# Kernel tuning notes

Hardware: AMD Instinct MI355X
Metric: run time of the kernel (lower is better)

Reference implementation:

```python
import jax, jax.numpy as jnp
import numpy as np

EMBED = 1024
HEADS = 16
HEAD_DIM = EMBED // HEADS
EXPANSION = 4
LN_EPS = 1e-5


def _layer_norm(x, gamma, beta):
    mu = jnp.mean(x, axis=-1, keepdims=True)
    var = jnp.mean(jnp.square(x - mu), axis=-1, keepdims=True)
    return (x - mu) * jax.lax.rsqrt(var + LN_EPS) * gamma + beta


def setup_inputs() -> dict:
    key = jax.random.key(0)
    ks = jax.random.split(key, 12)
    s = 0.02
    d_ff = EXPANSION * EMBED
    return {
        "x":  jax.random.normal(ks[0], (4, 4096, EMBED), dtype=jnp.float32),
        "Wq": jax.random.normal(ks[1], (EMBED, EMBED), dtype=jnp.float32) * s,
        "Wk": jax.random.normal(ks[2], (EMBED, EMBED), dtype=jnp.float32) * s,
        "Wv": jax.random.normal(ks[3], (EMBED, EMBED), dtype=jnp.float32) * s,
        "Wo": jax.random.normal(ks[4], (EMBED, EMBED), dtype=jnp.float32) * s,
        "bo": jnp.zeros((EMBED,), dtype=jnp.float32),
        "W1": jax.random.normal(ks[5], (EMBED, d_ff), dtype=jnp.float32) * s,
        "b1": jnp.zeros((d_ff,), dtype=jnp.float32),
        "W2": jax.random.normal(ks[6], (d_ff, EMBED), dtype=jnp.float32) * s,
        "b2": jnp.zeros((EMBED,), dtype=jnp.float32),
        "g1": jnp.ones((EMBED,), dtype=jnp.float32),
        "be1": jnp.zeros((EMBED,), dtype=jnp.float32),
        "g2": jnp.ones((EMBED,), dtype=jnp.float32),
        "be2": jnp.zeros((EMBED,), dtype=jnp.float32),
    }


def reference(x, Wq, Wk, Wv, Wo, bo, W1, b1, W2, b2, g1, be1, g2, be2):
    N, S, E = x.shape
    # projections (no bias on Q/K/V, matching nn.Linear(bias=False))
    q = (x @ Wq).reshape(N, S, HEADS, HEAD_DIM).transpose(0, 2, 1, 3)  # [N,H,S,D]
    k = (x @ Wk).reshape(N, S, HEADS, HEAD_DIM).transpose(0, 2, 1, 3)
    v = (x @ Wv).reshape(N, S, HEADS, HEAD_DIM).transpose(0, 2, 1, 3)
    # Faithful reproduction of the source einsums: after the permute, axis1 is
    # HEADS and axis2 is SEQ, so 'q'/'k' index heads and 'h' indexes seq here.
    energy = jnp.einsum('nqhd,nkhd->nqkh', q, k)            # [N,H,H,S]
    attn = jax.nn.softmax(energy / (HEAD_DIM ** 0.5), axis=3)
    out = jnp.einsum('nqkh,nvhd->nqhd', attn, v)            # sums over k AND v
    out = out.reshape(N, S, E)
    attn_out = out @ Wo + bo
    # residual + LN1 (dropout is identity in eval mode)
    h = _layer_norm(attn_out + x, g1, be1)
    # feed-forward
    ff = jax.nn.relu(h @ W1 + b1) @ W2 + b2
    y = _layer_norm(ff + h, g2, be2)
    return (y, k, v)
```

## Files before the change

### kernel.cpp

```cpp
#include <hip/hip_runtime.h>


#define S_LEN 4096
#define EMB   1024
#define NBATCH 4
#define NH    16
#define HD    64
#define DFF   4096
#define MROWS (NBATCH * S_LEN)

typedef __attribute__((ext_vector_type(8))) short s16x8;
typedef __attribute__((ext_vector_type(4))) float f32x4;

__device__ __forceinline__ float uas_f(unsigned u) { union { unsigned u; float f; } c; c.u = u; return c.f; }
__device__ __forceinline__ unsigned fas_u(float f) { union { float f; unsigned u; } c; c.f = f; return c.u; }
__device__ __forceinline__ short f2bf(float f) {
  unsigned u = fas_u(f);
  u += 0x7fffu + ((u >> 16) & 1u);
  return (short)(unsigned short)(u >> 16);
}
__device__ __forceinline__ float bf2f(short h) { return uas_f(((unsigned)(unsigned short)h) << 16); }
__device__ __forceinline__ float bflo(unsigned pk) { return uas_f(pk << 16); }
__device__ __forceinline__ float bfhi(unsigned pk) { return uas_f(pk & 0xffff0000u); }

__device__ __forceinline__ void gld16(const short* g, short* l) {
  __builtin_amdgcn_global_load_lds((const __attribute__((address_space(1))) void*)g,
                                   (__attribute__((address_space(3))) void*)l, 16, 0, 0);
}

#define BAR()   __builtin_amdgcn_s_barrier()
#define LGKM0() asm volatile("s_waitcnt lgkmcnt(0)" ::: "memory")
#define VMC8()  asm volatile("s_waitcnt vmcnt(8)" ::: "memory")

#define LOADA(BUFOFF, QH) do { \
  _Pragma("unroll") for (int mi = 0; mi < 4; ++mi) { \
    aR[mi][0] = *(const s16x8*)(aB + (BUFOFF) + (((QH)*8 + mi*2 + 0) << 10)); \
    aR[mi][1] = *(const s16x8*)(aB + (BUFOFF) + (((QH)*8 + mi*2 + 1) << 10)); } } while (0)

#define LOADB(BUFOFF, NH_) do { \
  _Pragma("unroll") for (int nf = 0; nf < 2; ++nf) { \
    bR[NH_][nf][0] = *(const s16x8*)(bB + (BUFOFF) + ((((NH_)*2 + nf)*2 + 0) << 10)); \
    bR[NH_][nf][1] = *(const s16x8*)(bB + (BUFOFF) + ((((NH_)*2 + nf)*2 + 1) << 10)); } } while (0)

#define MFMA16(QH, NH_) do { \
  _Pragma("unroll") for (int mi = 0; mi < 4; ++mi) \
  _Pragma("unroll") for (int nf = 0; nf < 2; ++nf) { \
    acc[(QH)*4+mi][(NH_)*2+nf] = __builtin_amdgcn_mfma_f32_16x16x32_bf16(aR[mi][0], bR[NH_][nf][0], acc[(QH)*4+mi][(NH_)*2+nf], 0, 0, 0); \
    acc[(QH)*4+mi][(NH_)*2+nf] = __builtin_amdgcn_mfma_f32_16x16x32_bf16(aR[mi][1], bR[NH_][nf][1], acc[(QH)*4+mi][(NH_)*2+nf], 0, 0, 0); } } while (0)

#define STG(PTR, OPOFF, BUFOFF, H, KOFF) do { \
  const short* _s = (PTR) + (KOFF); \
  char* _d = ldsc + (BUFOFF) + (OPOFF) + (H)*16384 + wq; \
  gld16(_s, (short*)_d); gld16(_s + 32, (short*)(_d + 1024)); } while (0)

template<bool OBF, bool RELU, bool BIAS>
__global__ __launch_bounds__(512, 2) void gemm2(const short* __restrict__ A,
                                                const short* __restrict__ BT,
                                                const float* __restrict__ bias,
                                                void* __restrict__ Cp,
                                                int N, int K, int lgx) {
  __shared__ __align__(16) char lds[131072];
  char* ldsc = &lds[0];
  const int t = threadIdx.x;
  const int lane = t & 63;
  const int wave = t >> 6;
  const int wr = wave >> 2, wc = wave & 3;

  const int nwg = gridDim.x;
  const int wg = blockIdx.x;
  const int sid = (wg & 7) * (nwg >> 3) + (wg >> 3);
  const int bx = sid & ((1 << lgx) - 1);
  const int by = sid >> lgx;
  const size_t m0 = (size_t)by * 256, n0 = (size_t)bx * 256;

  const int uc = lane ^ (((lane >> 5) & 1) << 1);
  const size_t arow = m0 + wave * 16 + (uc >> 2);
  const size_t brow = n0 + wave * 16 + (uc >> 2);
  const int csub = (uc & 3) << 3;
  const short* pA0 = A  + arow * K + csub;
  const short* pA1 = A  + (arow + 128) * K + csub;
  const short* pB0 = BT + brow * K + csub;
  const short* pB1 = BT + (brow + 128) * K + csub;
  const int wq = wave * 2048 + lane * 16;

  int ulane = ((lane & 15) << 6) | ((lane >> 4) << 4);
  ulane ^= ((lane >> 3) & 1) << 5;
  const char* aB = ldsc + (wr << 14) + ulane;
  const char* bB = ldsc + 32768 + (wc << 13) + ulane;

  s16x8 aR[4][2];
  s16x8 bR[2][2][2];
  f32x4 acc[8][4] = {};

  STG(pA0, 0,     0, 0, 0);       STG(pB0, 32768, 0, 0, 0);
  STG(pB1, 32768, 0, 1, 0);       STG(pA1, 0,     0, 1, 0);
  STG(pA0, 0,     65536, 0, 64);  STG(pB0, 32768, 65536, 0, 64);
  STG(pB1, 32768, 65536, 1, 64);  STG(pA1, 0,     65536, 1, 64);
  VMC8();
  BAR();

  const int niter = K >> 7;
  for (int it = 0; it < niter; ++it) {
    const int kb = it << 7;
    int k2 = kb + 128; if (k2 > K - 64) k2 = K - 64;
    int k3 = kb + 192; if (k3 > K - 64) k3 = K - 64;
    LOADA(0, 0); LOADB(0, 0);
    BAR(); LGKM0();
    __builtin_amdgcn_s_setprio(1); MFMA16(0, 0); __builtin_amdgcn_s_setprio(0);
    BAR();
    LOADB(0, 1);
    BAR(); LGKM0();
    __builtin_amdgcn_s_setprio(1); MFMA16(0, 1); __builtin_amdgcn_s_setprio(0);
    BAR();
    LOADA(0, 1);
    STG(pB0, 32768, 0, 0, k2); STG(pB1, 32768, 0, 1, k2);
    BAR(); LGKM0();
    __builtin_amdgcn_s_setprio(1); MFMA16(1, 1); __builtin_amdgcn_s_setprio(0);
    BAR();
    STG(pA0, 0, 0, 0, k2); STG(pA1, 0, 0, 1, k2);
    VMC8();
    BAR(); LGKM0();
    __builtin_amdgcn_s_setprio(1); MFMA16(1, 0); __builtin_amdgcn_s_setprio(0);
    BAR();
    LOADA(65536, 0); LOADB(65536, 0);
    BAR(); LGKM0();
    __builtin_amdgcn_s_setprio(1); MFMA16(0, 0); __builtin_amdgcn_s_setprio(0);
    BAR();
    LOADB(65536, 1);
    BAR(); LGKM0();
    __builtin_amdgcn_s_setprio(1); MFMA16(0, 1); __builtin_amdgcn_s_setprio(0);
    BAR();
    LOADA(65536, 1);
    STG(pB0, 32768, 65536, 0, k3); STG(pB1, 32768, 65536, 1, k3);
    BAR(); LGKM0();
    __builtin_amdgcn_s_setprio(1); MFMA16(1, 1); __builtin_amdgcn_s_setprio(0);
    BAR();
    STG(pA0, 0, 65536, 0, k3); STG(pA1, 0, 65536, 1, k3);
    VMC8();
    BAR(); LGKM0();
    __builtin_amdgcn_s_setprio(1); MFMA16(1, 0); __builtin_amdgcn_s_setprio(0);
    BAR();
  }

  const int r0 = (lane >> 4) << 2;
  const int c0 = lane & 15;
#pragma unroll
  for (int i = 0; i < 8; ++i) {
#pragma unroll
    for (int j = 0; j < 4; ++j) {
      const size_t row = m0 + (size_t)(wr * 128 + i * 16 + r0);
      const size_t col = n0 + (size_t)(wc * 64 + j * 16 + c0);
      float bv = 0.f;
      if (BIAS) bv = bias[col];
#pragma unroll
      for (int r = 0; r < 4; ++r) {
        float v = acc[i][j][r] + bv;
        if (RELU) v = fmaxf(v, 0.f);
        if (OBF) ((short*)Cp)[(row + r) * N + col] = f2bf(v);
        else     ((float*)Cp)[(row + r) * N + col] = v;
      }
    }
  }
}

__global__ __launch_bounds__(256) void cvtx_k(const float* __restrict__ in, short* __restrict__ out) {
  const size_t i = ((size_t)blockIdx.x * 256 + threadIdx.x) * 8;
  const float4 a = *(const float4*)(in + i);
  const float4 b = *(const float4*)(in + i + 4);
  s16x8 o;
  o[0] = f2bf(a.x); o[1] = f2bf(a.y); o[2] = f2bf(a.z); o[3] = f2bf(a.w);
  o[4] = f2bf(b.x); o[5] = f2bf(b.y); o[6] = f2bf(b.z); o[7] = f2bf(b.w);
  *(s16x8*)(out + i) = o;
}

__global__ void transpose_cvt_k(const float* __restrict__ W, short* __restrict__ WT, int K, int N) {
  __shared__ float tile[32][33];
  const int tx = threadIdx.x, ty = threadIdx.y;
  const int n0 = blockIdx.x * 32, k0 = blockIdx.y * 32;
#pragma unroll
  for (int i = 0; i < 32; i += 8)
    tile[ty + i][tx] = W[(size_t)(k0 + ty + i) * N + n0 + tx];
  __syncthreads();
#pragma unroll
  for (int i = 0; i < 32; i += 8)
    WT[(size_t)(n0 + ty + i) * K + k0 + tx] = f2bf(tile[tx][ty + i]);
}

__global__ __launch_bounds__(256) void energy_k(const short* __restrict__ q,
                                                const short* __restrict__ k,
                                                float* __restrict__ E) {
  __shared__ short qs[8][1024];
  __shared__ short ks[8][1024];
  const int t = threadIdx.x;
  const int blk = blockIdx.x;
  const int n = blk >> 9;
  const int s0 = (blk & 511) << 3;
  const size_t base = ((size_t)n * S_LEN + s0) * EMB;
#pragma unroll
  for (int i = 0; i < 4; ++i) {
    int idx = (t + i * 256) * 8;
    *(s16x8*)&qs[0][idx] = *(const s16x8*)&q[base + idx];
    *(s16x8*)&ks[0][idx] = *(const s16x8*)&k[base + idx];
  }
  __syncthreads();
  const int qh = t >> 4, kh = t & 15;
  const unsigned* qb = (const unsigned*)&qs[0][0] + qh * 32;
  const unsigned* kb = (const unsigned*)&ks[0][0] + kh * 32;
  float e[8];
#pragma unroll
  for (int sl = 0; sl < 8; ++sl) {
    const unsigned* qrow = qb + sl * 512;
    const unsigned* krow = kb + sl * 512;
    float acc = 0.f;
#pragma unroll 8
    for (int p = 0; p < 32; ++p) {
      int pp = (p + kh) & 31;
      unsigned qp = qrow[pp];
      unsigned kp = krow[pp];
      acc += bflo(qp) * bflo(kp) + bfhi(qp) * bfhi(kp);
    }
    e[sl] = acc * 0.125f;
  }
  float* dst = E + ((size_t)((n * NH + qh) * NH + kh)) * S_LEN + s0;
#pragma unroll
  for (int sl = 0; sl < 8; ++sl) dst[sl] = e[sl];
}

__global__ __launch_bounds__(256) void smstat_k(const float* __restrict__ E, float* __restrict__ mz) {
  __shared__ float red[8];
  const int t = threadIdx.x;
  const size_t r = blockIdx.x;
  const float* row = E + r * S_LEN;
  float vals[16];
  float m = -1e30f;
#pragma unroll
  for (int j = 0; j < 16; ++j) { vals[j] = row[t + j * 256]; m = fmaxf(m, vals[j]); }
#pragma unroll
  for (int off = 32; off > 0; off >>= 1) m = fmaxf(m, __shfl_down(m, off));
  if ((t & 63) == 0) red[t >> 6] = m;
  __syncthreads();
  m = fmaxf(fmaxf(red[0], red[1]), fmaxf(red[2], red[3]));
  float s = 0.f;
#pragma unroll
  for (int j = 0; j < 16; ++j) s += __expf(vals[j] - m);
#pragma unroll
  for (int off = 32; off > 0; off >>= 1) s += __shfl_down(s, off);
  if ((t & 63) == 0) red[4 + (t >> 6)] = s;
  __syncthreads();
  if (t == 0) {
    float Z = red[4] + red[5] + red[6] + red[7];
    mz[2 * r] = m;
    mz[2 * r + 1] = 1.f / Z;
  }
}

__global__ __launch_bounds__(256) void asum_k(const float* __restrict__ E, const float* __restrict__ mz,
                                              float* __restrict__ A) {
  const int nq = blockIdx.y;
  const int s = blockIdx.x * 256 + threadIdx.x;
  float a = 0.f;
#pragma unroll
  for (int kh = 0; kh < NH; ++kh) {
    const int r = nq * NH + kh;
    a += __expf(E[(size_t)r * S_LEN + s] - mz[2 * r]) * mz[2 * r + 1];
  }
  A[(size_t)nq * S_LEN + s] = a;
}

__global__ __launch_bounds__(256) void vsum_k(const short* __restrict__ v, float* __restrict__ Vs) {
  const size_t i = (size_t)blockIdx.x * 256 + threadIdx.x;
  const size_t ns = i >> 6;
  const int d = (int)(i & 63);
  const short* p = v + ns * EMB + d;
  float a = 0.f;
#pragma unroll
  for (int h = 0; h < NH; ++h) a += bf2f(p[h * 64]);
  Vs[i] = a;
}

__global__ __launch_bounds__(256) void kvout_k(const short* __restrict__ pre, float* __restrict__ out) {
  const size_t ns = blockIdx.x;
  const int n = (int)(ns >> 12), s = (int)(ns & 4095);
  const int t = threadIdx.x;
#pragma unroll
  for (int j = 0; j < 4; ++j) {
    int e = t + j * 256;
    int h = e >> 6, d = e & 63;
    out[(((size_t)n * NH + h) * S_LEN + s) * HD + d] = bf2f(pre[ns * EMB + e]);
  }
}

__global__ __launch_bounds__(256) void attnin_k(const float* __restrict__ A, const float* __restrict__ Vs,
                                                short* __restrict__ out) {
  __shared__ float Ash[16];
  const int t = threadIdx.x;
  const size_t ns = blockIdx.x;
  const int n = (int)(ns >> 12), s = (int)(ns & 4095);
  const int qh = s >> 8;
  const int h0 = (s & 255) * 16;
  if (t < 16) Ash[t] = A[((size_t)(n * NH + qh)) * S_LEN + h0 + t];
  __syncthreads();
  const float* vsrc = Vs + ((size_t)n * S_LEN + h0) * HD;
#pragma unroll
  for (int j = 0; j < 4; ++j) {
    int e = t + j * 256;
    out[ns * EMB + e] = f2bf(Ash[e >> 6] * vsrc[e]);
  }
}

template<bool WBF>
__global__ __launch_bounds__(256) void ln_k(const float* __restrict__ a, const float* __restrict__ b,
                                            const float* __restrict__ g, const float* __restrict__ be,
                                            float* __restrict__ out, short* __restrict__ obf) {
  __shared__ float red[8];
  const int t = threadIdx.x;
  const size_t r = blockIdx.x;
  const float4 va = *(const float4*)(a + r * EMB + t * 4);
  const float4 vb = *(const float4*)(b + r * EMB + t * 4);
  const float v0 = va.x + vb.x, v1 = va.y + vb.y, v2 = va.z + vb.z, v3 = va.w + vb.w;
  float s = v0 + v1 + v2 + v3;
  float q = v0 * v0 + v1 * v1 + v2 * v2 + v3 * v3;
#pragma unroll
  for (int off = 32; off > 0; off >>= 1) { s += __shfl_down(s, off); q += __shfl_down(q, off); }
  if ((t & 63) == 0) { red[t >> 6] = s; red[4 + (t >> 6)] = q; }
  __syncthreads();
  const float S = red[0] + red[1] + red[2] + red[3];
  const float Q = red[4] + red[5] + red[6] + red[7];
  const float mu = S * (1.f / EMB);
  const float var = Q * (1.f / EMB) - mu * mu;
  const float rstd = rsqrtf(var + 1e-5f);
  const float4 vg = *(const float4*)(g + t * 4);
  const float4 ve = *(const float4*)(be + t * 4);
  const float y0 = (v0 - mu) * rstd * vg.x + ve.x;
  const float y1 = (v1 - mu) * rstd * vg.y + ve.y;
  const float y2 = (v2 - mu) * rstd * vg.z + ve.z;
  const float y3 = (v3 - mu) * rstd * vg.w + ve.w;
  float4 yo; yo.x = y0; yo.y = y1; yo.z = y2; yo.w = y3;
  *(float4*)(out + r * EMB + t * 4) = yo;
  if (WBF) {
    short4 o; o.x = f2bf(y0); o.y = f2bf(y1); o.z = f2bf(y2); o.w = f2bf(y3);
    *(short4*)(obf + r * EMB + t * 4) = o;
  }
}

extern "C" void kernel_launch(void* const* d_in, const int* in_sizes, int n_in,
                              void* d_out, int out_size, void* d_ws, size_t ws_size,
                              hipStream_t stream) {
  const float* x   = (const float*)d_in[0];
  const float* Wq  = (const float*)d_in[1];
  const float* Wk  = (const float*)d_in[2];
  const float* Wv  = (const float*)d_in[3];
  const float* Wo  = (const float*)d_in[4];
  const float* bo  = (const float*)d_in[5];
  const float* W1  = (const float*)d_in[6];
  const float* b1  = (const float*)d_in[7];
  const float* W2  = (const float*)d_in[8];
  const float* b2  = (const float*)d_in[9];
  const float* g1  = (const float*)d_in[10];
  const float* be1 = (const float*)d_in[11];
  const float* g2  = (const float*)d_in[12];
  const float* be2 = (const float*)d_in[13];

  float* y    = (float*)d_out;
  float* kout = y + (size_t)MROWS * EMB;
  float* vout = kout + (size_t)MROWS * EMB;

  constexpr size_t MB = 1ull << 20;
  char* ws = (char*)d_ws;
  short* WqT     = (short*)(ws + 0 * MB);
  short* WkT     = (short*)(ws + 2 * MB);
  short* WvT     = (short*)(ws + 4 * MB);
  short* WoT     = (short*)(ws + 6 * MB);
  short* W1T     = (short*)(ws + 8 * MB);
  short* W2T     = (short*)(ws + 16 * MB);
  short* xbf     = (short*)(ws + 24 * MB);
  short* qpre    = (short*)(ws + 56 * MB);
  short* kpre    = (short*)(ws + 88 * MB);
  short* vpre    = (short*)(ws + 120 * MB);
  float* energy  = (float*)(ws + 152 * MB);
  float* mz      = (float*)(ws + 168 * MB);
  float* Avec    = (float*)(ws + 169 * MB);
  float* Vsb     = (float*)(ws + 170 * MB);
  short* attn_in = (short*)(ws + 174 * MB);
  float* attn_out= (float*)(ws + 206 * MB);
  float* hbuf    = (float*)(ws + 270 * MB);
  short* hbf     = (short*)(ws + 334 * MB);
  short* ff1     = (short*)(ws + 24 * MB);
  float* ff2     = (float*)(ws + 174 * MB);

  cvtx_k<<<8192, 256, 0, stream>>>(x, xbf);
  transpose_cvt_k<<<dim3(32, 32),  dim3(32, 8), 0, stream>>>(Wq, WqT, EMB, EMB);
  transpose_cvt_k<<<dim3(32, 32),  dim3(32, 8), 0, stream>>>(Wk, WkT, EMB, EMB);
  transpose_cvt_k<<<dim3(32, 32),  dim3(32, 8), 0, stream>>>(Wv, WvT, EMB, EMB);
  transpose_cvt_k<<<dim3(32, 32),  dim3(32, 8), 0, stream>>>(Wo, WoT, EMB, EMB);
  transpose_cvt_k<<<dim3(128, 32), dim3(32, 8), 0, stream>>>(W1, W1T, EMB, DFF);
  transpose_cvt_k<<<dim3(32, 128), dim3(32, 8), 0, stream>>>(W2, W2T, DFF, EMB);

  gemm2<true, false, false><<<256, 512, 0, stream>>>(xbf, WqT, nullptr, qpre, EMB, EMB, 2);
  gemm2<true, false, false><<<256, 512, 0, stream>>>(xbf, WkT, nullptr, kpre, EMB, EMB, 2);
  gemm2<true, false, false><<<256, 512, 0, stream>>>(xbf, WvT, nullptr, vpre, EMB, EMB, 2);

  energy_k<<<2048, 256, 0, stream>>>(qpre, kpre, energy);
  smstat_k<<<1024, 256, 0, stream>>>(energy, mz);
  asum_k<<<dim3(16, 64), 256, 0, stream>>>(energy, mz, Avec);
  vsum_k<<<4096, 256, 0, stream>>>(vpre, Vsb);
  kvout_k<<<16384, 256, 0, stream>>>(kpre, kout);
  kvout_k<<<16384, 256, 0, stream>>>(vpre, vout);
  attnin_k<<<16384, 256, 0, stream>>>(Avec, Vsb, attn_in);

  gemm2<false, false, true><<<256, 512, 0, stream>>>(attn_in, WoT, bo, attn_out, EMB, EMB, 2);
  ln_k<true><<<16384, 256, 0, stream>>>(attn_out, x, g1, be1, hbuf, hbf);

  gemm2<true, true, true><<<1024, 512, 0, stream>>>(hbf, W1T, b1, ff1, DFF, EMB, 4);
  gemm2<false, false, true><<<256, 512, 0, stream>>>(ff1, W2T, b2, ff2, EMB, DFF, 2);
  ln_k<false><<<16384, 256, 0, stream>>>(ff2, hbuf, g2, be2, y, nullptr);
}
```

Measured before the change: 888.5 us.

## Fuse residual adds and K/V output scatter into GEMM epilogues, restructure K-loop

Residual additions move into the GEMM epilogues, which now write bf16 pre-LayerNorm sums, so the LayerNorm kernels read a single bf16 stream instead of two fp32 tensors. The separate kvout kernels are removed and the K/V GEMMs write the fp32 head-major outputs directly. The main loop is rewritten as a KSTEP macro that issues more LDS loads up front, waits on partial lgkm counts, and peels the last iteration to skip out-of-range staging. The trade-offs are lower precision, since the residual and h are now rounded to bf16, and an uncoalesced scattered store in the K/V epilogue.

```diff
diff --git a/kernel.cpp b/kernel.cpp
--- a/kernel.cpp
+++ b/kernel.cpp
@@ -30,7 +30,9 @@
 
 #define BAR()   __builtin_amdgcn_s_barrier()
 #define LGKM0() asm volatile("s_waitcnt lgkmcnt(0)" ::: "memory")
+#define LGKM4() asm volatile("s_waitcnt lgkmcnt(4)" ::: "memory")
 #define VMC8()  asm volatile("s_waitcnt vmcnt(8)" ::: "memory")
+#define VMC0()  asm volatile("s_waitcnt vmcnt(0)" ::: "memory")
 
 #define LOADA(BUFOFF, QH) do { \
   _Pragma("unroll") for (int mi = 0; mi < 4; ++mi) { \
@@ -53,11 +55,32 @@
   char* _d = ldsc + (BUFOFF) + (OPOFF) + (H)*16384 + wq; \
   gld16(_s, (short*)_d); gld16(_s + 32, (short*)(_d + 1024)); } while (0)
 
-template<bool OBF, bool RELU, bool BIAS>
+#define PRIO1() __builtin_amdgcn_s_setprio(1)
+#define PRIO0() __builtin_amdgcn_s_setprio(0)
+
+#define KSTEP(BUF, KR, DOSTG, VMCT) do { \
+   \
+  LOADA(BUF, 0); LOADB(BUF, 0); LOADB(BUF, 1); \
+  PRIO1(); MFMA16(0, 0); PRIO0(); LGKM4(); BAR(); \
+   \
+  PRIO1(); MFMA16(0, 1); PRIO0(); LGKM0(); BAR(); \
+   \
+  LOADA(BUF, 1); \
+  if (DOSTG) { STG(pB0, 32768, BUF, 0, KR); STG(pB1, 32768, BUF, 1, KR); } \
+  PRIO1(); MFMA16(1, 1); PRIO0(); LGKM0(); BAR(); \
+   \
+  if (DOSTG) { STG(pA0, 0, BUF, 0, KR); STG(pA1, 0, BUF, 1, KR); } \
+  PRIO1(); MFMA16(1, 0); PRIO0(); LGKM0(); VMCT; BAR(); \
+} while (0)
+
+template<int CM, bool RELU, bool BIAS, bool KV, int RES>
 __global__ __launch_bounds__(512, 2) void gemm2(const short* __restrict__ A,
                                                 const short* __restrict__ BT,
                                                 const float* __restrict__ bias,
                                                 void* __restrict__ Cp,
+                                                float* __restrict__ kvp,
+                                                const float* __restrict__ resf,
+                                                const short* __restrict__ resb,
                                                 int N, int K, int lgx) {
   __shared__ __align__(16) char lds[131072];
   char* ldsc = &lds[0];
@@ -100,47 +123,13 @@
   BAR();
 
   const int niter = K >> 7;
-  for (int it = 0; it < niter; ++it) {
+  for (int it = 0; it < niter - 1; ++it) {
     const int kb = it << 7;
-    int k2 = kb + 128; if (k2 > K - 64) k2 = K - 64;
-    int k3 = kb + 192; if (k3 > K - 64) k3 = K - 64;
-    LOADA(0, 0); LOADB(0, 0);
-    BAR(); LGKM0();
-    __builtin_amdgcn_s_setprio(1); MFMA16(0, 0); __builtin_amdgcn_s_setprio(0);
-    BAR();
-    LOADB(0, 1);
-    BAR(); LGKM0();
-    __builtin_amdgcn_s_setprio(1); MFMA16(0, 1); __builtin_amdgcn_s_setprio(0);
-    BAR();
-    LOADA(0, 1);
-    STG(pB0, 32768, 0, 0, k2); STG(pB1, 32768, 0, 1, k2);
-    BAR(); LGKM0();
-    __builtin_amdgcn_s_setprio(1); MFMA16(1, 1); __builtin_amdgcn_s_setprio(0);
-    BAR();
-    STG(pA0, 0, 0, 0, k2); STG(pA1, 0, 0, 1, k2);
-    VMC8();
-    BAR(); LGKM0();
-    __builtin_amdgcn_s_setprio(1); MFMA16(1, 0); __builtin_amdgcn_s_setprio(0);
-    BAR();
-    LOADA(65536, 0); LOADB(65536, 0);
-    BAR(); LGKM0();
-    __builtin_amdgcn_s_setprio(1); MFMA16(0, 0); __builtin_amdgcn_s_setprio(0);
-    BAR();
-    LOADB(65536, 1);
-    BAR(); LGKM0();
-    __builtin_amdgcn_s_setprio(1); MFMA16(0, 1); __builtin_amdgcn_s_setprio(0);
-    BAR();
-    LOADA(65536, 1);
-    STG(pB0, 32768, 65536, 0, k3); STG(pB1, 32768, 65536, 1, k3);
-    BAR(); LGKM0();
-    __builtin_amdgcn_s_setprio(1); MFMA16(1, 1); __builtin_amdgcn_s_setprio(0);
-    BAR();
-    STG(pA0, 0, 65536, 0, k3); STG(pA1, 0, 65536, 1, k3);
-    VMC8();
-    BAR(); LGKM0();
-    __builtin_amdgcn_s_setprio(1); MFMA16(1, 0); __builtin_amdgcn_s_setprio(0);
-    BAR();
-  }
+    KSTEP(0,     kb + 128, 1, VMC8());
+    KSTEP(65536, kb + 192, 1, VMC8());
+  }
+  KSTEP(0,     0, 0, VMC0());
+  KSTEP(65536, 0, 0, ((void)0));
 
   const int r0 = (lane >> 4) << 2;
   const int c0 = lane & 15;
@@ -155,9 +144,17 @@
 #pragma unroll
       for (int r = 0; r < 4; ++r) {
         float v = acc[i][j][r] + bv;
+        if (RES == 1) v += resf[(row + r) * N + col];
+        if (RES == 2) v += bf2f(resb[(row + r) * N + col]);
         if (RELU) v = fmaxf(v, 0.f);
-        if (OBF) ((short*)Cp)[(row + r) * N + col] = f2bf(v);
-        else     ((float*)Cp)[(row + r) * N + col] = v;
+        if (CM) ((short*)Cp)[(row + r) * N + col] = f2bf(v);
+        else    ((float*)Cp)[(row + r) * N + col] = v;
+        if (KV) {
+          const size_t rr = row + r;
+          const int n = (int)(rr >> 12), s = (int)(rr & 4095);
+          const int h = (int)(col >> 6), d = (int)(col & 63);
+          kvp[(((size_t)n * NH + h) * S_LEN + s) * HD + d] = v;
+        }
       }
     }
   }
@@ -278,18 +275,6 @@
   Vs[i] = a;
 }
 
-__global__ __launch_bounds__(256) void kvout_k(const short* __restrict__ pre, float* __restrict__ out) {
-  const size_t ns = blockIdx.x;
-  const int n = (int)(ns >> 12), s = (int)(ns & 4095);
-  const int t = threadIdx.x;
-#pragma unroll
-  for (int j = 0; j < 4; ++j) {
-    int e = t + j * 256;
-    int h = e >> 6, d = e & 63;
-    out[(((size_t)n * NH + h) * S_LEN + s) * HD + d] = bf2f(pre[ns * EMB + e]);
-  }
-}
-
 __global__ __launch_bounds__(256) void attnin_k(const float* __restrict__ A, const float* __restrict__ Vs,
                                                 short* __restrict__ out) {
   __shared__ float Ash[16];
@@ -308,16 +293,15 @@
   }
 }
 
-template<bool WBF>
-__global__ __launch_bounds__(256) void ln_k(const float* __restrict__ a, const float* __restrict__ b,
+template<bool OBF>
+__global__ __launch_bounds__(256) void ln_s(const short* __restrict__ in,
                                             const float* __restrict__ g, const float* __restrict__ be,
-                                            float* __restrict__ out, short* __restrict__ obf) {
+                                            void* __restrict__ outp) {
   __shared__ float red[8];
   const int t = threadIdx.x;
   const size_t r = blockIdx.x;
-  const float4 va = *(const float4*)(a + r * EMB + t * 4);
-  const float4 vb = *(const float4*)(b + r * EMB + t * 4);
-  const float v0 = va.x + vb.x, v1 = va.y + vb.y, v2 = va.z + vb.z, v3 = va.w + vb.w;
+  const short4 a = *(const short4*)(in + r * EMB + t * 4);
+  const float v0 = bf2f(a.x), v1 = bf2f(a.y), v2 = bf2f(a.z), v3 = bf2f(a.w);
   float s = v0 + v1 + v2 + v3;
   float q = v0 * v0 + v1 * v1 + v2 * v2 + v3 * v3;
 #pragma unroll
@@ -335,11 +319,12 @@
   const float y1 = (v1 - mu) * rstd * vg.y + ve.y;
   const float y2 = (v2 - mu) * rstd * vg.z + ve.z;
   const float y3 = (v3 - mu) * rstd * vg.w + ve.w;
-  float4 yo; yo.x = y0; yo.y = y1; yo.z = y2; yo.w = y3;
-  *(float4*)(out + r * EMB + t * 4) = yo;
-  if (WBF) {
+  if (OBF) {
     short4 o; o.x = f2bf(y0); o.y = f2bf(y1); o.z = f2bf(y2); o.w = f2bf(y3);
-    *(short4*)(obf + r * EMB + t * 4) = o;
+    *(short4*)((short*)outp + r * EMB + t * 4) = o;
+  } else {
+    float4 yo; yo.x = y0; yo.y = y1; yo.z = y2; yo.w = y3;
+    *(float4*)((float*)outp + r * EMB + t * 4) = yo;
   }
 }
 
@@ -382,11 +367,10 @@
   float* Avec    = (float*)(ws + 169 * MB);
   float* Vsb     = (float*)(ws + 170 * MB);
   short* attn_in = (short*)(ws + 174 * MB);
-  float* attn_out= (float*)(ws + 206 * MB);
-  float* hbuf    = (float*)(ws + 270 * MB);
+  short* attn_res= (short*)(ws + 206 * MB);
   short* hbf     = (short*)(ws + 334 * MB);
   short* ff1     = (short*)(ws + 24 * MB);
-  float* ff2     = (float*)(ws + 174 * MB);
+  short* ff2res  = (short*)(ws + 174 * MB);
 
   cvtx_k<<<8192, 256, 0, stream>>>(x, xbf);
   transpose_cvt_k<<<dim3(32, 32),  dim3(32, 8), 0, stream>>>(Wq, WqT, EMB, EMB);
@@ -396,22 +380,20 @@
   transpose_cvt_k<<<dim3(128, 32), dim3(32, 8), 0, stream>>>(W1, W1T, EMB, DFF);
   transpose_cvt_k<<<dim3(32, 128), dim3(32, 8), 0, stream>>>(W2, W2T, DFF, EMB);
 
-  gemm2<true, false, false><<<256, 512, 0, stream>>>(xbf, WqT, nullptr, qpre, EMB, EMB, 2);
-  gemm2<true, false, false><<<256, 512, 0, stream>>>(xbf, WkT, nullptr, kpre, EMB, EMB, 2);
-  gemm2<true, false, false><<<256, 512, 0, stream>>>(xbf, WvT, nullptr, vpre, EMB, EMB, 2);
+  gemm2<1, false, false, false, 0><<<256, 512, 0, stream>>>(xbf, WqT, nullptr, qpre, nullptr, nullptr, nullptr, EMB, EMB, 2);
+  gemm2<1, false, false, true,  0><<<256, 512, 0, stream>>>(xbf, WkT, nullptr, kpre, kout,    nullptr, nullptr, EMB, EMB, 2);
+  gemm2<1, false, false, true,  0><<<256, 512, 0, stream>>>(xbf, WvT, nullptr, vpre, vout,    nullptr, nullptr, EMB, EMB, 2);
 
   energy_k<<<2048, 256, 0, stream>>>(qpre, kpre, energy);
   smstat_k<<<1024, 256, 0, stream>>>(energy, mz);
   asum_k<<<dim3(16, 64), 256, 0, stream>>>(energy, mz, Avec);
   vsum_k<<<4096, 256, 0, stream>>>(vpre, Vsb);
-  kvout_k<<<16384, 256, 0, stream>>>(kpre, kout);
-  kvout_k<<<16384, 256, 0, stream>>>(vpre, vout);
   attnin_k<<<16384, 256, 0, stream>>>(Avec, Vsb, attn_in);
 
-  gemm2<false, false, true><<<256, 512, 0, stream>>>(attn_in, WoT, bo, attn_out, EMB, EMB, 2);
-  ln_k<true><<<16384, 256, 0, stream>>>(attn_out, x, g1, be1, hbuf, hbf);
-
-  gemm2<true, true, true><<<1024, 512, 0, stream>>>(hbf, W1T, b1, ff1, DFF, EMB, 4);
-  gemm2<false, false, true><<<256, 512, 0, stream>>>(ff1, W2T, b2, ff2, EMB, DFF, 2);
-  ln_k<false><<<16384, 256, 0, stream>>>(ff2, hbuf, g2, be2, y, nullptr);
-}
+  gemm2<1, false, true, false, 1><<<256, 512, 0, stream>>>(attn_in, WoT, bo, attn_res, nullptr, x, nullptr, EMB, EMB, 2);
+  ln_s<true><<<16384, 256, 0, stream>>>(attn_res, g1, be1, hbf);
+
+  gemm2<1, true,  true, false, 0><<<1024, 512, 0, stream>>>(hbf, W1T, b1, ff1, nullptr, nullptr, nullptr, DFF, EMB, 4);
+  gemm2<1, false, true, false, 2><<<256, 512, 0, stream>>>(ff1, W2T, b2, ff2res, nullptr, nullptr, hbf, EMB, DFF, 2);
+  ln_s<false><<<16384, 256, 0, stream>>>(ff2res, g2, be2, y);
+}
```

New measurement: 809.5 us. 8.9% less time.
